# Performance work log

Measured on AMD Instinct MI355X. Metric: run time of the kernel, lower is better.

## Reference

```python
import jax, jax.numpy as jnp
import numpy as np

N, E, IN_DIM, OUT_DIM = 12288, 6144, 256, 256


def setup_inputs() -> dict:
    key = jax.random.key(0)
    k1, k2, k3, k4, k5 = jax.random.split(key, 5)
    x = jax.random.normal(k1, (N, IN_DIM), dtype=jnp.float32)
    # incidence-like matrix (dense, values in [0,1))
    H = jax.random.uniform(k2, (N, E), dtype=jnp.float32)
    # degree-normalizer diagonals: positive entries on the diagonal
    dv = jax.random.uniform(k3, (N,), dtype=jnp.float32, minval=0.1, maxval=1.0)
    de = jax.random.uniform(k4, (E,), dtype=jnp.float32, minval=0.1, maxval=1.0)
    D_v_neg_sqrt = jnp.diag(dv)
    D_e_neg = jnp.diag(de)
    # Linear params (xavier-like weight, zero bias)
    W = jax.random.normal(k5, (IN_DIM, OUT_DIM), dtype=jnp.float32) * (1.0 / np.sqrt(IN_DIM))
    b = jnp.zeros((OUT_DIM,), dtype=jnp.float32)
    return {"x": x, "H": H, "D_v_neg_sqrt": D_v_neg_sqrt, "D_e_neg": D_e_neg, "W": W, "b": b}


def reference(x, H, D_v_neg_sqrt, D_e_neg, W, b):
    # x_transformed = Linear(x)
    x_t = x @ W + b                      # [N, out]
    x_norm = D_v_neg_sqrt @ x_t          # [N, out]
    x_he = H.T @ x_norm                  # [E, out]
    x_he_norm = D_e_neg @ x_he           # [E, out]
    x_node = H @ x_he_norm               # [N, out]
    out = D_v_neg_sqrt @ x_node          # [N, out]
    # dropout is identity in eval mode
    return out
```

## Files before the change

### kernel.cpp

```cpp
#include <hip/hip_runtime.h>

#define NN 12288
#define NE 6144
#define ND 256

typedef __attribute__((ext_vector_type(8))) short short8;
typedef __attribute__((ext_vector_type(4))) float f32x4;
typedef unsigned short u16;
typedef unsigned int u32;

__device__ inline u16 f2bf(float f) {
  union { float f; u32 u; } v; v.f = f;
  u32 r = v.u + 0x7fffu + ((v.u >> 16) & 1u);
  return (u16)(r >> 16);
}

__device__ inline void gll16(const void* g, void* l) {
  __builtin_amdgcn_global_load_lds(
      (const __attribute__((address_space(1))) u32*)g,
      (__attribute__((address_space(3))) u32*)l, 16, 0, 0);
}

__device__ inline void stage_B4(const u16* __restrict__ Bg, int ldb, int k0,
                                u16* __restrict__ Blds) {
  const int w = threadIdx.x >> 6;
  const int lane = threadIdx.x & 63;
  const int dd = lane >> 2, p = lane & 3;
#pragma unroll
  for (int s = 0; s < 4; ++s) {
    const int dbase = (w * 4 + s) * 16;
    const int n = dbase + dd;
    const int c = (p - (n >> 1)) & 3;
    gll16(Bg + (size_t)n * ldb + k0 + c * 8, Blds + dbase * 32);
  }
}

__device__ inline void stage_B8(const u16* __restrict__ Bg, int ldb, int k0,
                                u16* __restrict__ Blds) {
  const int w = threadIdx.x >> 6;
  const int lane = threadIdx.x & 63;
  const int dd = lane >> 2, p = lane & 3;
#pragma unroll
  for (int s = 0; s < 2; ++s) {
    const int dbase = (w * 2 + s) * 16;
    const int n = dbase + dd;
    const int c = (p - (n >> 1)) & 3;
    gll16(Bg + (size_t)n * ldb + k0 + c * 8, Blds + dbase * 32);
  }
}

__device__ inline short8 load_B(const u16* __restrict__ Blds, int n, int quad) {
  const int p = (quad + (n >> 1)) & 3;
  return *(const short8*)(Blds + n * 32 + p * 8);
}

__device__ inline void compute_tile(const u16* __restrict__ Al, int arow0,
                                    const u16* __restrict__ Bl, int bcol0,
                                    int ln, int quad, f32x4 (&acc)[4][4]) {
  short8 af[4];
#pragma unroll
  for (int mt = 0; mt < 4; ++mt)
    af[mt] = *(const short8*)(Al + (arow0 + mt * 16 + ln) * 40 + quad * 8);
#pragma unroll
  for (int nt = 0; nt < 4; ++nt) {
    short8 bf = load_B(Bl, bcol0 + nt * 16 + ln, quad);
#pragma unroll
    for (int mt = 0; mt < 4; ++mt)
      acc[nt][mt] = __builtin_amdgcn_mfma_f32_16x16x32_bf16(af[mt], bf, acc[nt][mt], 0, 0, 0);
  }
}

__device__ inline short8 pack8(float4 f0, float4 f1) {
  short8 av;
  av[0] = (short)f2bf(f0.x); av[1] = (short)f2bf(f0.y);
  av[2] = (short)f2bf(f0.z); av[3] = (short)f2bf(f0.w);
  av[4] = (short)f2bf(f1.x); av[5] = (short)f2bf(f1.y);
  av[6] = (short)f2bf(f1.z); av[7] = (short)f2bf(f1.w);
  return av;
}

__global__ __launch_bounds__(256) void k_xform(
    const float* __restrict__ x, const u16* __restrict__ Wt,
    const float* __restrict__ b, const float* __restrict__ dv,
    u16* __restrict__ xnt) {
  __shared__ u16 Alds[64 * 40];
  __shared__ u16 Blds[256 * 32];
  const int tid = threadIdx.x;
  const int w = tid >> 6, lane = tid & 63, ln = lane & 15, quad = lane >> 4;
  const int m0 = blockIdx.x * 64;
  const int am = tid >> 2, ac = (tid & 3) * 8;
  f32x4 acc[4][4] = {};
  for (int kt = 0; kt < ND / 32; ++kt) {
    const int k0 = kt * 32;
    __syncthreads();
    stage_B4(Wt, ND, k0, Blds);
    const float4* pa = (const float4*)(x + (size_t)(m0 + am) * ND + k0 + ac);
    *(short8*)(Alds + am * 40 + ac) = pack8(pa[0], pa[1]);
    __syncthreads();
    compute_tile(Alds, 0, Blds, w * 64, ln, quad, acc);
  }
#pragma unroll
  for (int nt = 0; nt < 4; ++nt) {
    const int d = w * 64 + nt * 16 + ln;
    const float bb = b[d];
#pragma unroll
    for (int mt = 0; mt < 4; ++mt) {
      const int vb = m0 + mt * 16 + quad * 4;
      f32x4 a = acc[nt][mt];
      union { u16 h[4]; uint2 u; } pk;
#pragma unroll
      for (int r = 0; r < 4; ++r) pk.h[r] = f2bf(dv[vb + r] * (a[r] + bb));
      *(uint2*)(xnt + (size_t)d * NN + vb) = pk.u;
    }
  }
}

template <int NC>
__global__ __launch_bounds__(512) void k_gemm1s(
    const float* __restrict__ H, const u16* __restrict__ xnt,
    float* __restrict__ P1) {
  constexpr int KLEN = NN / NC;
  __shared__ u16 Alds[128 * 40];
  __shared__ u16 Blds[256 * 32];
  const int tid = threadIdx.x;
  const int w = tid >> 6, lane = tid & 63, ln = lane & 15, quad = lane >> 4;
  const int wn = w & 3, wm = w >> 2;
  const int e0 = blockIdx.x * 128;
  const int kbase = blockIdx.y * KLEN;
  const int ec = tid & 31, vp = tid >> 5;
  f32x4 acc[4][4] = {};
  for (int kt = 0; kt < KLEN / 32; ++kt) {
    const int k0 = kbase + kt * 32;
    __syncthreads();
    stage_B8(xnt, NN, k0, Blds);
    const int v = k0 + vp * 2;
    const float4 h0 = *(const float4*)(H + (size_t)v * NE + e0 + ec * 4);
    const float4 h1 = *(const float4*)(H + (size_t)(v + 1) * NE + e0 + ec * 4);
    const float a0[4] = {h0.x, h0.y, h0.z, h0.w};
    const float a1[4] = {h1.x, h1.y, h1.z, h1.w};
#pragma unroll
    for (int j = 0; j < 4; ++j) {
      u32 pk = (u32)f2bf(a0[j]) | ((u32)f2bf(a1[j]) << 16);
      *(u32*)(Alds + (ec * 4 + j) * 40 + vp * 2) = pk;
    }
    __syncthreads();
    compute_tile(Alds, wm * 64, Blds, wn * 64, ln, quad, acc);
  }
  float* P = P1 + (size_t)blockIdx.y * NE * ND;
#pragma unroll
  for (int nt = 0; nt < 4; ++nt) {
    const int d = wn * 64 + nt * 16 + ln;
#pragma unroll
    for (int mt = 0; mt < 4; ++mt) {
      const int eb = e0 + wm * 64 + mt * 16 + quad * 4;
      f32x4 a = acc[nt][mt];
#pragma unroll
      for (int r = 0; r < 4; ++r)
        P[(size_t)(eb + r) * ND + d] = a[r];
    }
  }
}

template <int NC>
__global__ __launch_bounds__(256) void k_red1(
    const float* __restrict__ P1, const float* __restrict__ de,
    u16* __restrict__ xhet) {
  const int tid = threadIdx.x;
  const int e0 = blockIdx.x * 16;
  union { u16 h[16]; uint4 q[2]; } pk;
#pragma unroll
  for (int i = 0; i < 16; ++i) {
    float s = 0.f;
#pragma unroll
    for (int c = 0; c < NC; ++c)
      s += P1[(size_t)c * NE * ND + (size_t)(e0 + i) * ND + tid];
    pk.h[i] = f2bf(de[e0 + i] * s);
  }
  uint4* dst = (uint4*)(xhet + (size_t)tid * NE + e0);
  dst[0] = pk.q[0];
  dst[1] = pk.q[1];
}

template <int NC>
__global__ __launch_bounds__(512) void k_gemm2s(
    const float* __restrict__ H, const u16* __restrict__ xhet,
    float* __restrict__ P2) {
  constexpr int KLEN = NE / NC;
  __shared__ u16 Alds[128 * 40];
  __shared__ u16 Blds[256 * 32];
  const int tid = threadIdx.x;
  const int w = tid >> 6, lane = tid & 63, ln = lane & 15, quad = lane >> 4;
  const int wn = w & 3, wm = w >> 2;
  const int m0 = blockIdx.x * 128;
  const int kbase = blockIdx.y * KLEN;
  const int am = tid >> 2, ac = (tid & 3) * 8;
  f32x4 acc[4][4] = {};
  for (int kt = 0; kt < KLEN / 32; ++kt) {
    const int k0 = kbase + kt * 32;
    __syncthreads();
    stage_B8(xhet, NE, k0, Blds);
    const float4* pa = (const float4*)(H + (size_t)(m0 + am) * NE + k0 + ac);
    *(short8*)(Alds + am * 40 + ac) = pack8(pa[0], pa[1]);
    __syncthreads();
    compute_tile(Alds, wm * 64, Blds, wn * 64, ln, quad, acc);
  }
  float* P = P2 + (size_t)blockIdx.y * NN * ND;
#pragma unroll
  for (int nt = 0; nt < 4; ++nt) {
    const int d = wn * 64 + nt * 16 + ln;
#pragma unroll
    for (int mt = 0; mt < 4; ++mt) {
      const int vb = m0 + wm * 64 + mt * 16 + quad * 4;
      f32x4 a = acc[nt][mt];
#pragma unroll
      for (int r = 0; r < 4; ++r)
        P[(size_t)(vb + r) * ND + d] = a[r];
    }
  }
}

template <int NC>
__global__ __launch_bounds__(256) void k_red2(
    const float* __restrict__ P2, const float* __restrict__ dv,
    float* __restrict__ out) {
  const int tid = threadIdx.x;
  const int v0 = blockIdx.x * 16;
#pragma unroll
  for (int i = 0; i < 16; ++i) {
    float s = 0.f;
#pragma unroll
    for (int c = 0; c < NC; ++c)
      s += P2[(size_t)c * NN * ND + (size_t)(v0 + i) * ND + tid];
    out[(size_t)(v0 + i) * ND + tid] = dv[v0 + i] * s;
  }
}

__global__ __launch_bounds__(256) void k_prep(
    const float* __restrict__ W, const float* __restrict__ Dv,
    const float* __restrict__ De, u16* __restrict__ Wt,
    float* __restrict__ dv, float* __restrict__ de) {
  const int t = blockIdx.x * 256 + threadIdx.x;
  const int d = t >> 8, k = t & 255;
  Wt[d * 256 + k] = f2bf(W[k * 256 + d]);
  if (t < NN) dv[t] = Dv[(size_t)t * (NN + 1)];
  if (t < NE) de[t] = De[(size_t)t * (NE + 1)];
}

extern "C" void kernel_launch(void* const* d_in, const int* in_sizes, int n_in,
                              void* d_out, int out_size, void* d_ws, size_t ws_size,
                              hipStream_t stream) {
  const float* x  = (const float*)d_in[0];
  const float* H  = (const float*)d_in[1];
  const float* Dv = (const float*)d_in[2];
  const float* De = (const float*)d_in[3];
  const float* W  = (const float*)d_in[4];
  const float* b  = (const float*)d_in[5];
  float* out = (float*)d_out;
  char* ws = (char*)d_ws;
  u16* xnt   = (u16*)ws;
  u16* xhet  = (u16*)(ws + 6291456);
  u16* Wt    = (u16*)(ws + 9437184);
  float* dv  = (float*)(ws + 9568256);
  float* de  = (float*)(ws + 9617408);
  float* P1  = (float*)(ws + 9641984);
  float* P2  = P1;

  hipLaunchKernelGGL(k_prep,       dim3(256), dim3(256), 0, stream, W, Dv, De, Wt, dv, de);
  hipLaunchKernelGGL(k_xform,      dim3(NN / 64), dim3(256), 0, stream, x, Wt, b, dv, xnt);
  hipLaunchKernelGGL(k_gemm1s<16>, dim3(NE / 128, 16), dim3(512), 0, stream, H, xnt, P1);
  hipLaunchKernelGGL(k_red1<16>,   dim3(NE / 16), dim3(256), 0, stream, P1, de, xhet);
  hipLaunchKernelGGL(k_gemm2s<8>,  dim3(NN / 128, 8), dim3(512), 0, stream, H, xhet, P2);
  hipLaunchKernelGGL(k_red2<8>,    dim3(NN / 16), dim3(256), 0, stream, P2, dv, out);
}
```

Measured before the change: 1.074 ms.

## Double-buffer LDS tiles in both split-K GEMMs to overlap loads with MFMA

Both big GEMM kernels now keep two LDS buffers for the A and B tiles. The next tile's H rows and global-to-LDS B staging are issued before computing on the current tile, with explicit waitcnt and barriers. This hides global memory latency behind the matrix-core work instead of serialising load and compute each iteration. It doubles LDS usage per block, which may reduce occupancy, and the hand-tuned vmcnt values depend on the exact number of outstanding loads.

```diff
diff --git a/kernel.cpp b/kernel.cpp
--- a/kernel.cpp
+++ b/kernel.cpp
@@ -120,8 +120,9 @@
     const float* __restrict__ H, const u16* __restrict__ xnt,
     float* __restrict__ P1) {
   constexpr int KLEN = NN / NC;
-  __shared__ u16 Alds[128 * 40];
-  __shared__ u16 Blds[256 * 32];
+  constexpr int NT = KLEN / 32;
+  __shared__ u16 Alds[2][128 * 40];
+  __shared__ u16 Blds[2][256 * 32];
   const int tid = threadIdx.x;
   const int w = tid >> 6, lane = tid & 63, ln = lane & 15, quad = lane >> 4;
   const int wn = w & 3, wm = w >> 2;
@@ -129,23 +130,50 @@
   const int kbase = blockIdx.y * KLEN;
   const int ec = tid & 31, vp = tid >> 5;
   f32x4 acc[4][4] = {};
-  for (int kt = 0; kt < KLEN / 32; ++kt) {
-    const int k0 = kbase + kt * 32;
-    __syncthreads();
-    stage_B8(xnt, NN, k0, Blds);
-    const int v = k0 + vp * 2;
-    const float4 h0 = *(const float4*)(H + (size_t)v * NE + e0 + ec * 4);
-    const float4 h1 = *(const float4*)(H + (size_t)(v + 1) * NE + e0 + ec * 4);
-    const float a0[4] = {h0.x, h0.y, h0.z, h0.w};
-    const float a1[4] = {h1.x, h1.y, h1.z, h1.w};
+  const float* aH = H + (size_t)(kbase + vp * 2) * NE + e0 + ec * 4;
+
+  {
+    float4 a0 = *(const float4*)(aH);
+    float4 a1 = *(const float4*)(aH + NE);
+    stage_B8(xnt, NN, kbase, Blds[0]);
+    const float p0[4] = {a0.x, a0.y, a0.z, a0.w};
+    const float p1[4] = {a1.x, a1.y, a1.z, a1.w};
 #pragma unroll
     for (int j = 0; j < 4; ++j) {
-      u32 pk = (u32)f2bf(a0[j]) | ((u32)f2bf(a1[j]) << 16);
-      *(u32*)(Alds + (ec * 4 + j) * 40 + vp * 2) = pk;
-    }
-    __syncthreads();
-    compute_tile(Alds, wm * 64, Blds, wn * 64, ln, quad, acc);
-  }
+      u32 pk = (u32)f2bf(p0[j]) | ((u32)f2bf(p1[j]) << 16);
+      *(u32*)(Alds[0] + (ec * 4 + j) * 40 + vp * 2) = pk;
+    }
+    asm volatile("s_waitcnt vmcnt(0) lgkmcnt(0)" ::: "memory");
+    __builtin_amdgcn_s_barrier();
+    __builtin_amdgcn_sched_barrier(0);
+  }
+  int cur = 0;
+  for (int t = 0; t < NT - 1; ++t) {
+    const int nxt = cur ^ 1;
+    const float* ap = aH + (size_t)((t + 1) * 32) * NE;
+    float4 ma0 = *(const float4*)(ap);
+    float4 ma1 = *(const float4*)(ap + NE);
+    stage_B8(xnt, NN, kbase + (t + 1) * 32, Blds[nxt]);
+    asm volatile("s_waitcnt vmcnt(4) lgkmcnt(0)" ::: "memory");
+    __builtin_amdgcn_s_barrier();
+    __builtin_amdgcn_sched_barrier(0);
+    compute_tile(Alds[cur], wm * 64, Blds[cur], wn * 64, ln, quad, acc);
+    __builtin_amdgcn_s_barrier();
+    __builtin_amdgcn_sched_barrier(0);
+    const float q0[4] = {ma0.x, ma0.y, ma0.z, ma0.w};
+    const float q1[4] = {ma1.x, ma1.y, ma1.z, ma1.w};
+#pragma unroll
+    for (int j = 0; j < 4; ++j) {
+      u32 pk = (u32)f2bf(q0[j]) | ((u32)f2bf(q1[j]) << 16);
+      *(u32*)(Alds[nxt] + (ec * 4 + j) * 40 + vp * 2) = pk;
+    }
+    cur = nxt;
+  }
+  asm volatile("s_waitcnt vmcnt(0) lgkmcnt(0)" ::: "memory");
+  __builtin_amdgcn_s_barrier();
+  __builtin_amdgcn_sched_barrier(0);
+  compute_tile(Alds[cur], wm * 64, Blds[cur], wn * 64, ln, quad, acc);
+
   float* P = P1 + (size_t)blockIdx.y * NE * ND;
 #pragma unroll
   for (int nt = 0; nt < 4; ++nt) {
@@ -186,8 +214,9 @@
     const float* __restrict__ H, const u16* __restrict__ xhet,
     float* __restrict__ P2) {
   constexpr int KLEN = NE / NC;
-  __shared__ u16 Alds[128 * 40];
-  __shared__ u16 Blds[256 * 32];
+  constexpr int NT = KLEN / 32;
+  __shared__ u16 Alds[2][128 * 40];
+  __shared__ u16 Blds[2][256 * 32];
   const int tid = threadIdx.x;
   const int w = tid >> 6, lane = tid & 63, ln = lane & 15, quad = lane >> 4;
   const int wn = w & 3, wm = w >> 2;
@@ -195,15 +224,38 @@
   const int kbase = blockIdx.y * KLEN;
   const int am = tid >> 2, ac = (tid & 3) * 8;
   f32x4 acc[4][4] = {};
-  for (int kt = 0; kt < KLEN / 32; ++kt) {
-    const int k0 = kbase + kt * 32;
-    __syncthreads();
-    stage_B8(xhet, NE, k0, Blds);
-    const float4* pa = (const float4*)(H + (size_t)(m0 + am) * NE + k0 + ac);
-    *(short8*)(Alds + am * 40 + ac) = pack8(pa[0], pa[1]);
-    __syncthreads();
-    compute_tile(Alds, wm * 64, Blds, wn * 64, ln, quad, acc);
-  }
+  const float* aH = H + (size_t)(m0 + am) * NE + kbase + ac;
+
+  {
+    float4 a0 = *(const float4*)(aH);
+    float4 a1 = *(const float4*)(aH + 4);
+    stage_B8(xhet, NE, kbase, Blds[0]);
+    *(short8*)(Alds[0] + am * 40 + ac) = pack8(a0, a1);
+    asm volatile("s_waitcnt vmcnt(0) lgkmcnt(0)" ::: "memory");
+    __builtin_amdgcn_s_barrier();
+    __builtin_amdgcn_sched_barrier(0);
+  }
+  int cur = 0;
+  for (int t = 0; t < NT - 1; ++t) {
+    const int nxt = cur ^ 1;
+    const float* ap = aH + (t + 1) * 32;
+    float4 ma0 = *(const float4*)(ap);
+    float4 ma1 = *(const float4*)(ap + 4);
+    stage_B8(xhet, NE, kbase + (t + 1) * 32, Blds[nxt]);
+    asm volatile("s_waitcnt vmcnt(4) lgkmcnt(0)" ::: "memory");
+    __builtin_amdgcn_s_barrier();
+    __builtin_amdgcn_sched_barrier(0);
+    compute_tile(Alds[cur], wm * 64, Blds[cur], wn * 64, ln, quad, acc);
+    __builtin_amdgcn_s_barrier();
+    __builtin_amdgcn_sched_barrier(0);
+    *(short8*)(Alds[nxt] + am * 40 + ac) = pack8(ma0, ma1);
+    cur = nxt;
+  }
+  asm volatile("s_waitcnt vmcnt(0) lgkmcnt(0)" ::: "memory");
+  __builtin_amdgcn_s_barrier();
+  __builtin_amdgcn_sched_barrier(0);
+  compute_tile(Alds[cur], wm * 64, Blds[cur], wn * 64, ln, quad, acc);
+
   float* P = P2 + (size_t)blockIdx.y * NN * ND;
 #pragma unroll
   for (int nt = 0; nt < 4; ++nt) {
```

New measurement: 1.068 ms. No clear change (-0.6%).
